# Kernel tuning notes

Measured on AMD Instinct MI355X. Metric: run time of the kernel, lower is better.

Reference implementation:

```python
import jax, jax.numpy as jnp
import numpy as np

D_MODEL = 1024
NUM_EXPERTS = 8
TOP_K = 2
B, S = 1, 2048


def setup_inputs() -> dict:
    key = jax.random.key(0)
    ks = jax.random.split(key, 8)
    sd = 1.0 / np.sqrt(D_MODEL)
    x = jax.random.normal(ks[0], (B, S, D_MODEL), dtype=jnp.float32)
    gate_w = jax.random.normal(ks[1], (D_MODEL, NUM_EXPERTS), dtype=jnp.float32) * sd
    gate_b = jnp.zeros((NUM_EXPERTS,), dtype=jnp.float32)
    w1 = jax.random.normal(ks[2], (NUM_EXPERTS, D_MODEL, 8 * D_MODEL), dtype=jnp.float32) * sd
    b1 = jnp.zeros((NUM_EXPERTS, 8 * D_MODEL), dtype=jnp.float32)
    w2 = jax.random.normal(ks[3], (NUM_EXPERTS, 4 * D_MODEL, D_MODEL), dtype=jnp.float32) * (1.0 / np.sqrt(4 * D_MODEL))
    b2 = jnp.zeros((NUM_EXPERTS, D_MODEL), dtype=jnp.float32)
    return {"x": x, "gate_w": gate_w, "gate_b": gate_b, "w1": w1, "b1": b1, "w2": w2, "b2": b2}


def reference(x, gate_w, gate_b, w1, b1, w2, b2):
    # Gating: top-k logits, softmax over the selected k
    gate_logits = jnp.einsum('bsd,de->bse', x, gate_w) + gate_b          # [B,S,E]
    weights, indices = jax.lax.top_k(gate_logits, TOP_K)                  # [B,S,K]
    weights = jax.nn.softmax(weights, axis=-1)

    # Dense all-expert compute (matches original masked-sum math; dropout in eval)
    h = jnp.einsum('bsd,edh->ebsh', x, w1) + b1[:, None, None, :]         # [E,B,S,8D]
    xh, gh = jnp.split(h, 2, axis=-1)                                     # each [E,B,S,4D]
    act = jax.nn.silu(gh) * xh
    out_e = jnp.einsum('ebsf,efd->ebsd', act, w2) + b2[:, None, None, :]  # [E,B,S,D]

    # Combine: gather the top-k expert outputs per token and weight-sum
    out_e = jnp.transpose(out_e, (1, 2, 0, 3))                            # [B,S,E,D]
    sel = jnp.take_along_axis(out_e, indices[..., None], axis=2)          # [B,S,K,D]
    return jnp.sum(sel * weights[..., None], axis=2)                      # [B,S,D]
```

## Files before the change

kernel.cpp:

```cpp
#include <hip/hip_runtime.h>
#include <hip/hip_bf16.h>

#define S 2048
#define D 1024
#define NE 8
#define HF 4096
#define HH 8192
#define BK 32
#define ACT_ROWS 4224
#define MAXRB 40

typedef __attribute__((ext_vector_type(8))) __bf16 bf16x8;
typedef __attribute__((ext_vector_type(4))) float f32x4;

__device__ __forceinline__ unsigned cvtpk(float lo, float hi) {
  unsigned r;
  asm("v_cvt_pk_bf16_f32 %0, %1, %2" : "=v"(r) : "v"(lo), "v"(hi));
  return r;
}
__device__ __forceinline__ unsigned bf16b(float f) {
  unsigned b = __float_as_uint(f);
  return (b + 0x7fffu + ((b >> 16) & 1u)) >> 16;
}
__device__ __forceinline__ void gll16(const ushort* g, ushort* l) {
  __builtin_amdgcn_global_load_lds(
      (const __attribute__((address_space(1))) void*)g,
      (__attribute__((address_space(3))) void*)l, 16, 0, 0);
}

__global__ __launch_bounds__(256) void gate_kernel(
    const float* __restrict__ x, const float* __restrict__ gw,
    const float* __restrict__ gb, ushort* __restrict__ xb,
    int* __restrict__ mi0, int* __restrict__ mi1,
    float* __restrict__ mw0, float* __restrict__ mw1) {
  const int t = blockIdx.x;
  const int l = threadIdx.x;
  const float4 xv = ((const float4*)(x + (size_t)t * D))[l];
  uint2 wv = {cvtpk(xv.x, xv.y), cvtpk(xv.z, xv.w)};
  ((uint2*)(xb + (size_t)t * D))[l] = wv;

  float xa[4] = {xv.x, xv.y, xv.z, xv.w};
  float acc[NE];
#pragma unroll
  for (int e = 0; e < NE; ++e) acc[e] = 0.f;
  const float* g0 = gw + (size_t)(4 * l) * NE;
#pragma unroll
  for (int j = 0; j < 4; ++j)
#pragma unroll
    for (int e = 0; e < NE; ++e) acc[e] += xa[j] * g0[j * NE + e];
#pragma unroll
  for (int e = 0; e < NE; ++e) {
    float v = acc[e];
#pragma unroll
    for (int off = 32; off > 0; off >>= 1) v += __shfl_xor(v, off);
    acc[e] = v;
  }
  __shared__ float sm[4][NE];
  const int wid = l >> 6;
  if ((l & 63) == 0) {
#pragma unroll
    for (int e = 0; e < NE; ++e) sm[wid][e] = acc[e];
  }
  __syncthreads();
  if (l == 0) {
    float lg[NE];
#pragma unroll
    for (int e = 0; e < NE; ++e)
      lg[e] = sm[0][e] + sm[1][e] + sm[2][e] + sm[3][e] + gb[e];
    int i0 = 0; float m0 = lg[0];
#pragma unroll
    for (int e = 1; e < NE; ++e) if (lg[e] > m0) { m0 = lg[e]; i0 = e; }
    int i1 = -1; float m1 = -3.4e38f;
#pragma unroll
    for (int e = 0; e < NE; ++e) if (e != i0 && lg[e] > m1) { m1 = lg[e]; i1 = e; }
    float p = __expf(m1 - m0);
    float inv = 1.f / (1.f + p);
    mi0[t] = i0; mi1[t] = i1;
    mw0[t] = inv; mw1[t] = p * inv;
  }
}

__global__ __launch_bounds__(1024) void route_kernel(
    const int* __restrict__ mi0, const int* __restrict__ mi1,
    int* __restrict__ counts, int* __restrict__ basep, int* __restrict__ list_tok,
    int* __restrict__ mr0, int* __restrict__ mr1,
    int* __restrict__ rb_e, int* __restrict__ rb_row0, int* __restrict__ rb_n) {
  __shared__ int cnt[NE];
  __shared__ int cur[NE];
  const int t = threadIdx.x;
  if (t < NE) cnt[t] = 0;
  __syncthreads();
  const int e0a = mi0[t], e1a = mi1[t];
  const int e0b = mi0[t + 1024], e1b = mi1[t + 1024];
  atomicAdd(&cnt[e0a], 1); atomicAdd(&cnt[e1a], 1);
  atomicAdd(&cnt[e0b], 1); atomicAdd(&cnt[e1b], 1);
  __syncthreads();
  if (t == 0) {
    int s = 0;
#pragma unroll
    for (int e = 0; e < NE; ++e) { basep[e] = s; cur[e] = s; s += cnt[e]; }
    basep[NE] = s;
    int nrb = 0;
    for (int e = 0; e < NE; ++e)
      for (int r0 = 0; r0 < cnt[e]; r0 += 128) {
        rb_e[nrb] = e; rb_row0[nrb] = r0; ++nrb;
      }
    *rb_n = nrb;
  }
  if (t < NE) counts[t] = cnt[t];
  __syncthreads();
  int r;
  r = atomicAdd(&cur[e0a], 1); list_tok[r] = t; mr0[t] = r;
  r = atomicAdd(&cur[e1a], 1); list_tok[r] = t; mr1[t] = r;
  r = atomicAdd(&cur[e0b], 1); list_tok[r] = t + 1024; mr0[t + 1024] = r;
  r = atomicAdd(&cur[e1b], 1); list_tok[r] = t + 1024; mr1[t + 1024] = r;
}

__global__ __launch_bounds__(256) void gemm1_kernel(
    const ushort* __restrict__ xb, const float* __restrict__ w1,
    const float* __restrict__ b1, const int* __restrict__ counts,
    const int* __restrict__ basep, const int* __restrict__ list_tok,
    const int* __restrict__ rb_e, const int* __restrict__ rb_row0,
    const int* __restrict__ rb_n, ushort* __restrict__ act_buf) {
  const int rb = blockIdx.y;
  if (rb >= *rb_n) return;
  const int e = rb_e[rb];
  const int row0 = rb_row0[rb];
  const int cnt = counts[e];
  const int jt = blockIdx.x * 64;
  const float* __restrict__ Wf = w1 + (size_t)e * D * HH;
  const int gbase = basep[e];

  __shared__ ushort As[2][128][BK];
  __shared__ unsigned Bs[2][32][68];

  const int tid = threadIdx.x;
  const int w = tid >> 6;
  const int i = tid & 63;

  const int rA0 = w * 32 + (i >> 2);
  const int rA1 = rA0 + 16;
  int s0 = row0 + rA0; if (s0 >= cnt) s0 = cnt - 1;
  int s1 = row0 + rA1; if (s1 >= cnt) s1 = cnt - 1;
  const ushort* pa0 = xb + (size_t)list_tok[gbase + s0] * D + (i & 3) * 8;
  const ushort* pa1 = xb + (size_t)list_tok[gbase + s1] * D + (i & 3) * 8;

  const int kp = tid >> 4;
  const int n4 = (tid & 15) * 4;
  const float* pBx = Wf + (size_t)(2 * kp) * HH + jt + n4;
  const float* pBg = pBx + HF;

  const int wm = (w >> 1) * 64;
  const int wn = (w & 1) * 32;
  const int lr = i & 15;
  const int kg = i >> 4;

  f32x4 acc[2][4][2] = {};

  {
    float4 x0 = *(const float4*)(pBx);
    float4 x1 = *(const float4*)(pBx + HH);
    float4 g0 = *(const float4*)(pBg);
    float4 g1 = *(const float4*)(pBg + HH);
    uint4 ux = {cvtpk(x0.x, x1.x), cvtpk(x0.y, x1.y), cvtpk(x0.z, x1.z), cvtpk(x0.w, x1.w)};
    uint4 ug = {cvtpk(g0.x, g1.x), cvtpk(g0.y, g1.y), cvtpk(g0.z, g1.z), cvtpk(g0.w, g1.w)};
    *(uint4*)&Bs[0][kp][n4] = ux;
    *(uint4*)&Bs[0][16 + kp][n4] = ug;
  }
  gll16(pa0, &As[0][w * 32][0]);
  gll16(pa1, &As[0][w * 32 + 16][0]);
  __syncthreads();

  int cur = 0;
#pragma unroll 1
  for (int it = 0; it < D / BK; ++it) {
    const bool pf = (it + 1 < D / BK);
    float4 x0, x1, g0, g1;
    if (pf) {
      const size_t koff = (size_t)(it + 1) * BK * HH;
      x0 = *(const float4*)(pBx + koff);
      x1 = *(const float4*)(pBx + koff + HH);
      g0 = *(const float4*)(pBg + koff);
      g1 = *(const float4*)(pBg + koff + HH);
      const int ko = (it + 1) * BK;
      gll16(pa0 + ko, &As[cur ^ 1][w * 32][0]);
      gll16(pa1 + ko, &As[cur ^ 1][w * 32 + 16][0]);
    }
    bf16x8 af[4], bfr[2][2];
#pragma unroll
    for (int mi = 0; mi < 4; ++mi)
      af[mi] = *(const bf16x8*)&As[cur][wm + mi * 16 + lr][kg * 8];
#pragma unroll
    for (int h = 0; h < 2; ++h)
#pragma unroll
      for (int ni = 0; ni < 2; ++ni) {
        const int col = wn + ni * 16 + lr;
        uint4 tv;
        tv.x = Bs[cur][h * 16 + kg * 4 + 0][col];
        tv.y = Bs[cur][h * 16 + kg * 4 + 1][col];
        tv.z = Bs[cur][h * 16 + kg * 4 + 2][col];
        tv.w = Bs[cur][h * 16 + kg * 4 + 3][col];
        bfr[h][ni] = *(const bf16x8*)&tv;
      }
#pragma unroll
    for (int h = 0; h < 2; ++h)
#pragma unroll
      for (int mi = 0; mi < 4; ++mi)
#pragma unroll
        for (int ni = 0; ni < 2; ++ni)
          acc[h][mi][ni] = __builtin_amdgcn_mfma_f32_16x16x32_bf16(af[mi], bfr[h][ni],
                                                                   acc[h][mi][ni], 0, 0, 0);
    if (pf) {
      uint4 ux = {cvtpk(x0.x, x1.x), cvtpk(x0.y, x1.y), cvtpk(x0.z, x1.z), cvtpk(x0.w, x1.w)};
      uint4 ug = {cvtpk(g0.x, g1.x), cvtpk(g0.y, g1.y), cvtpk(g0.z, g1.z), cvtpk(g0.w, g1.w)};
      *(uint4*)&Bs[cur ^ 1][kp][n4] = ux;
      *(uint4*)&Bs[cur ^ 1][16 + kp][n4] = ug;
    }
    __syncthreads();
    cur ^= 1;
  }

#pragma unroll
  for (int mi = 0; mi < 4; ++mi)
#pragma unroll
    for (int ni = 0; ni < 2; ++ni) {
      const int c = jt + wn + ni * 16 + lr;
      const float bx = b1[(size_t)e * HH + c];
      const float bg = b1[(size_t)e * HH + HF + c];
      f32x4 vx = acc[0][mi][ni];
      f32x4 vg = acc[1][mi][ni];
#pragma unroll
      for (int q = 0; q < 4; ++q) {
        const int slot = row0 + wm + mi * 16 + kg * 4 + q;
        if (slot < cnt) {
          float xv = vx[q] + bx;
          float g = vg[q] + bg;
          float a = g / (1.f + __expf(-g)) * xv;
          act_buf[(size_t)(gbase + slot) * HF + c] = (ushort)bf16b(a);
        }
      }
    }
}

__global__ __launch_bounds__(256) void gemm2_kernel(
    const ushort* __restrict__ act_buf, const float* __restrict__ w2,
    const int* __restrict__ counts, const int* __restrict__ basep,
    const int* __restrict__ rb_e, const int* __restrict__ rb_row0,
    const int* __restrict__ rb_n, ushort* __restrict__ oe) {
  const int rb = blockIdx.y;
  if (rb >= *rb_n) return;
  const int e = rb_e[rb];
  const int row0 = rb_row0[rb];
  const int cnt = counts[e];
  const int split = blockIdx.z;
  const int jt = blockIdx.x * 128;
  const float* __restrict__ Wf = w2 + (size_t)e * HF * D;
  const int gbase = basep[e];
  const size_t kbase = (size_t)split * (HF / 2);

  __shared__ ushort As[2][128][BK];
  __shared__ unsigned Bs[2][16][132];

  const int tid = threadIdx.x;
  const int w = tid >> 6;
  const int i = tid & 63;

  const int rA0 = w * 32 + (i >> 2);
  const ushort* pa0 = act_buf + (size_t)(gbase + row0 + rA0) * HF + kbase + (i & 3) * 8;
  const ushort* pa1 = pa0 + (size_t)16 * HF;

  const int grp = tid >> 5;
  const int n4 = (tid & 31) * 4;
  const float* pB0 = Wf + (kbase + 2 * grp) * D + jt + n4;
  const float* pB1 = pB0 + (size_t)16 * D;

  const int wm = (w >> 1) * 64;
  const int wn = (w & 1) * 64;
  const int lr = i & 15;
  const int kg = i >> 4;

  f32x4 acc[4][4] = {};

  {
    float4 a0 = *(const float4*)(pB0);
    float4 a1 = *(const float4*)(pB0 + D);
    float4 c0 = *(const float4*)(pB1);
    float4 c1 = *(const float4*)(pB1 + D);
    uint4 u0 = {cvtpk(a0.x, a1.x), cvtpk(a0.y, a1.y), cvtpk(a0.z, a1.z), cvtpk(a0.w, a1.w)};
    uint4 u1 = {cvtpk(c0.x, c1.x), cvtpk(c0.y, c1.y), cvtpk(c0.z, c1.z), cvtpk(c0.w, c1.w)};
    *(uint4*)&Bs[0][grp][n4] = u0;
    *(uint4*)&Bs[0][8 + grp][n4] = u1;
  }
  gll16(pa0, &As[0][w * 32][0]);
  gll16(pa1, &As[0][w * 32 + 16][0]);
  __syncthreads();

  int cur = 0;
#pragma unroll 1
  for (int it = 0; it < (HF / 2) / BK; ++it) {
    const bool pf = (it + 1 < (HF / 2) / BK);
    float4 a0, a1, c0, c1;
    if (pf) {
      const size_t koff = (size_t)(it + 1) * BK * D;
      a0 = *(const float4*)(pB0 + koff);
      a1 = *(const float4*)(pB0 + koff + D);
      c0 = *(const float4*)(pB1 + koff);
      c1 = *(const float4*)(pB1 + koff + D);
      const int ko = (it + 1) * BK;
      gll16(pa0 + ko, &As[cur ^ 1][w * 32][0]);
      gll16(pa1 + ko, &As[cur ^ 1][w * 32 + 16][0]);
    }
    bf16x8 af[4], bfr[4];
#pragma unroll
    for (int mi = 0; mi < 4; ++mi)
      af[mi] = *(const bf16x8*)&As[cur][wm + mi * 16 + lr][kg * 8];
#pragma unroll
    for (int ni = 0; ni < 4; ++ni) {
      const int col = wn + ni * 16 + lr;
      uint4 tv;
      tv.x = Bs[cur][kg * 4 + 0][col];
      tv.y = Bs[cur][kg * 4 + 1][col];
      tv.z = Bs[cur][kg * 4 + 2][col];
      tv.w = Bs[cur][kg * 4 + 3][col];
      bfr[ni] = *(const bf16x8*)&tv;
    }
#pragma unroll
    for (int mi = 0; mi < 4; ++mi)
#pragma unroll
      for (int ni = 0; ni < 4; ++ni)
        acc[mi][ni] = __builtin_amdgcn_mfma_f32_16x16x32_bf16(af[mi], bfr[ni],
                                                              acc[mi][ni], 0, 0, 0);
    if (pf) {
      uint4 u0 = {cvtpk(a0.x, a1.x), cvtpk(a0.y, a1.y), cvtpk(a0.z, a1.z), cvtpk(a0.w, a1.w)};
      uint4 u1 = {cvtpk(c0.x, c1.x), cvtpk(c0.y, c1.y), cvtpk(c0.z, c1.z), cvtpk(c0.w, c1.w)};
      *(uint4*)&Bs[cur ^ 1][grp][n4] = u0;
      *(uint4*)&Bs[cur ^ 1][8 + grp][n4] = u1;
    }
    __syncthreads();
    cur ^= 1;
  }

#pragma unroll
  for (int mi = 0; mi < 4; ++mi)
#pragma unroll
    for (int ni = 0; ni < 4; ++ni) {
      f32x4 v = acc[mi][ni];
#pragma unroll
      for (int q = 0; q < 4; ++q) {
        const int slot = row0 + wm + mi * 16 + kg * 4 + q;
        if (slot < cnt)
          oe[((size_t)split * ACT_ROWS + gbase + slot) * D + jt + wn + ni * 16 + lr] =
              (ushort)bf16b(v[q]);
      }
    }
}

__global__ void combine_kernel(const ushort* __restrict__ oe,
                               const int* __restrict__ mr0, const int* __restrict__ mr1,
                               const float* __restrict__ mw0, const float* __restrict__ mw1,
                               const int* __restrict__ mi0, const int* __restrict__ mi1,
                               const float* __restrict__ b2, float* __restrict__ out) {
  const int t = blockIdx.x;
  const int l = threadIdx.x;
  const float w0 = mw0[t], w1 = mw1[t];
  const int r0 = mr0[t], r1 = mr1[t];
  float a0[4] = {0.f, 0.f, 0.f, 0.f}, a1[4] = {0.f, 0.f, 0.f, 0.f};
#pragma unroll
  for (int s = 0; s < 2; ++s) {
    uint2 u0 = *(const uint2*)(oe + ((size_t)s * ACT_ROWS + r0) * D + l * 4);
    uint2 u1 = *(const uint2*)(oe + ((size_t)s * ACT_ROWS + r1) * D + l * 4);
    a0[0] += __uint_as_float(u0.x << 16);
    a0[1] += __uint_as_float(u0.x & 0xffff0000u);
    a0[2] += __uint_as_float(u0.y << 16);
    a0[3] += __uint_as_float(u0.y & 0xffff0000u);
    a1[0] += __uint_as_float(u1.x << 16);
    a1[1] += __uint_as_float(u1.x & 0xffff0000u);
    a1[2] += __uint_as_float(u1.y << 16);
    a1[3] += __uint_as_float(u1.y & 0xffff0000u);
  }
  float4 c0 = ((const float4*)(b2 + (size_t)mi0[t] * D))[l];
  float4 c1 = ((const float4*)(b2 + (size_t)mi1[t] * D))[l];
  float4 r;
  r.x = w0 * (a0[0] + c0.x) + w1 * (a1[0] + c1.x);
  r.y = w0 * (a0[1] + c0.y) + w1 * (a1[1] + c1.y);
  r.z = w0 * (a0[2] + c0.z) + w1 * (a1[2] + c1.z);
  r.w = w0 * (a0[3] + c0.w) + w1 * (a1[3] + c1.w);
  ((float4*)(out + (size_t)t * D))[l] = r;
}

extern "C" void kernel_launch(void* const* d_in, const int* in_sizes, int n_in,
                              void* d_out, int out_size, void* d_ws, size_t ws_size,
                              hipStream_t stream) {
  const float* x  = (const float*)d_in[0];
  const float* gw = (const float*)d_in[1];
  const float* gb = (const float*)d_in[2];
  const float* w1 = (const float*)d_in[3];
  const float* b1 = (const float*)d_in[4];
  const float* w2 = (const float*)d_in[5];
  const float* b2 = (const float*)d_in[6];
  float* out = (float*)d_out;

  char* ws = (char*)d_ws;
  int*   counts   = (int*)(ws + 0);
  int*   basep    = (int*)(ws + 64);
  int*   rb_n     = (int*)(ws + 128);
  int*   rb_e     = (int*)(ws + 192);
  int*   rb_row0  = (int*)(ws + 384);
  int*   mi0      = (int*)(ws + 1024);
  int*   mi1      = (int*)(ws + 1024 + 1 * 8192);
  int*   mr0      = (int*)(ws + 1024 + 2 * 8192);
  int*   mr1      = (int*)(ws + 1024 + 3 * 8192);
  float* mw0      = (float*)(ws + 1024 + 4 * 8192);
  float* mw1      = (float*)(ws + 1024 + 5 * 8192);
  int*   list_tok = (int*)(ws + 1024 + 6 * 8192);
  ushort* xb      = (ushort*)(ws + 66560);
  ushort* act_buf = (ushort*)(ws + 4260864);
  ushort* oe      = (ushort*)(ws + 38863872);

  gate_kernel<<<S, 256, 0, stream>>>(x, gw, gb, xb, mi0, mi1, mw0, mw1);
  route_kernel<<<1, 1024, 0, stream>>>(mi0, mi1, counts, basep, list_tok, mr0, mr1,
                                       rb_e, rb_row0, rb_n);
  gemm1_kernel<<<dim3(64, MAXRB), 256, 0, stream>>>(xb, w1, b1, counts, basep, list_tok,
                                                    rb_e, rb_row0, rb_n, act_buf);
  gemm2_kernel<<<dim3(8, MAXRB, 2), 256, 0, stream>>>(act_buf, w2, counts, basep,
                                                      rb_e, rb_row0, rb_n, oe);
  combine_kernel<<<S, 256, 0, stream>>>(oe, mr0, mr1, mw0, mw1, mi0, mi1, b2, out);
}
```

Before: 266.1 us.

## Enlarge gemm1 row tile to 256 with 512 threads to halve weight re-reads

Routes gemm1 through a second row-block list with 256-row blocks and launches it with 512 threads, so each block covers twice as many token rows per expert. Each w1 fp32 tile is loaded and converted to bf16 once per 256 rows instead of once per 128, and the B-tile load is split so each half of the threads handles either the x or the gate half. This is meant to cut redundant global weight traffic and conversion work. In exchange the grid has fewer blocks, LDS per block grows, and experts with few tokens pad more rows per block.

New measurement: 261.4 us (median of 2 runs). No clear change (-1.8%).

```diff
diff --git a/kernel.cpp b/kernel.cpp
--- a/kernel.cpp
+++ b/kernel.cpp
@@ -9,6 +9,7 @@
 #define BK 32
 #define ACT_ROWS 4224
 #define MAXRB 40
+#define MAXRB2 24
 
 typedef __attribute__((ext_vector_type(8))) __bf16 bf16x8;
 typedef __attribute__((ext_vector_type(4))) float f32x4;
@@ -84,7 +85,8 @@
     const int* __restrict__ mi0, const int* __restrict__ mi1,
     int* __restrict__ counts, int* __restrict__ basep, int* __restrict__ list_tok,
     int* __restrict__ mr0, int* __restrict__ mr1,
-    int* __restrict__ rb_e, int* __restrict__ rb_row0, int* __restrict__ rb_n) {
+    int* __restrict__ rb_e, int* __restrict__ rb_row0, int* __restrict__ rb_n,
+    int* __restrict__ rb2_e, int* __restrict__ rb2_row0, int* __restrict__ rb2_n) {
   __shared__ int cnt[NE];
   __shared__ int cur[NE];
   const int t = threadIdx.x;
@@ -100,12 +102,17 @@
 #pragma unroll
     for (int e = 0; e < NE; ++e) { basep[e] = s; cur[e] = s; s += cnt[e]; }
     basep[NE] = s;
-    int nrb = 0;
-    for (int e = 0; e < NE; ++e)
+    int nrb = 0, nrb2 = 0;
+    for (int e = 0; e < NE; ++e) {
       for (int r0 = 0; r0 < cnt[e]; r0 += 128) {
         rb_e[nrb] = e; rb_row0[nrb] = r0; ++nrb;
       }
+      for (int r0 = 0; r0 < cnt[e]; r0 += 256) {
+        rb2_e[nrb2] = e; rb2_row0[nrb2] = r0; ++nrb2;
+      }
+    }
     *rb_n = nrb;
+    *rb2_n = nrb2;
   }
   if (t < NE) counts[t] = cnt[t];
   __syncthreads();
@@ -116,22 +123,22 @@
   r = atomicAdd(&cur[e1b], 1); list_tok[r] = t + 1024; mr1[t + 1024] = r;
 }
 
-__global__ __launch_bounds__(256) void gemm1_kernel(
+__global__ __launch_bounds__(512) void gemm1_kernel(
     const ushort* __restrict__ xb, const float* __restrict__ w1,
     const float* __restrict__ b1, const int* __restrict__ counts,
     const int* __restrict__ basep, const int* __restrict__ list_tok,
-    const int* __restrict__ rb_e, const int* __restrict__ rb_row0,
-    const int* __restrict__ rb_n, ushort* __restrict__ act_buf) {
+    const int* __restrict__ rb2_e, const int* __restrict__ rb2_row0,
+    const int* __restrict__ rb2_n, ushort* __restrict__ act_buf) {
   const int rb = blockIdx.y;
-  if (rb >= *rb_n) return;
-  const int e = rb_e[rb];
-  const int row0 = rb_row0[rb];
+  if (rb >= *rb2_n) return;
+  const int e = rb2_e[rb];
+  const int row0 = rb2_row0[rb];
   const int cnt = counts[e];
   const int jt = blockIdx.x * 64;
   const float* __restrict__ Wf = w1 + (size_t)e * D * HH;
   const int gbase = basep[e];
 
-  __shared__ ushort As[2][128][BK];
+  __shared__ ushort As[2][256][BK];
   __shared__ unsigned Bs[2][32][68];
 
   const int tid = threadIdx.x;
@@ -145,10 +152,10 @@
   const ushort* pa0 = xb + (size_t)list_tok[gbase + s0] * D + (i & 3) * 8;
   const ushort* pa1 = xb + (size_t)list_tok[gbase + s1] * D + (i & 3) * 8;
 
-  const int kp = tid >> 4;
+  const int half = tid >> 8;
+  const int kp = (tid >> 4) & 15;
   const int n4 = (tid & 15) * 4;
-  const float* pBx = Wf + (size_t)(2 * kp) * HH + jt + n4;
-  const float* pBg = pBx + HF;
+  const float* pB = Wf + (size_t)(2 * kp) * HH + jt + n4 + half * HF;
 
   const int wm = (w >> 1) * 64;
   const int wn = (w & 1) * 32;
@@ -158,14 +165,11 @@
   f32x4 acc[2][4][2] = {};
 
   {
-    float4 x0 = *(const float4*)(pBx);
-    float4 x1 = *(const float4*)(pBx + HH);
-    float4 g0 = *(const float4*)(pBg);
-    float4 g1 = *(const float4*)(pBg + HH);
-    uint4 ux = {cvtpk(x0.x, x1.x), cvtpk(x0.y, x1.y), cvtpk(x0.z, x1.z), cvtpk(x0.w, x1.w)};
-    uint4 ug = {cvtpk(g0.x, g1.x), cvtpk(g0.y, g1.y), cvtpk(g0.z, g1.z), cvtpk(g0.w, g1.w)};
-    *(uint4*)&Bs[0][kp][n4] = ux;
-    *(uint4*)&Bs[0][16 + kp][n4] = ug;
+    float4 b0v = *(const float4*)(pB);
+    float4 b1v = *(const float4*)(pB + HH);
+    uint4 u = {cvtpk(b0v.x, b1v.x), cvtpk(b0v.y, b1v.y),
+               cvtpk(b0v.z, b1v.z), cvtpk(b0v.w, b1v.w)};
+    *(uint4*)&Bs[0][half * 16 + kp][n4] = u;
   }
   gll16(pa0, &As[0][w * 32][0]);
   gll16(pa1, &As[0][w * 32 + 16][0]);
@@ -175,13 +179,11 @@
 #pragma unroll 1
   for (int it = 0; it < D / BK; ++it) {
     const bool pf = (it + 1 < D / BK);
-    float4 x0, x1, g0, g1;
+    float4 b0v, b1v;
     if (pf) {
       const size_t koff = (size_t)(it + 1) * BK * HH;
-      x0 = *(const float4*)(pBx + koff);
-      x1 = *(const float4*)(pBx + koff + HH);
-      g0 = *(const float4*)(pBg + koff);
-      g1 = *(const float4*)(pBg + koff + HH);
+      b0v = *(const float4*)(pB + koff);
+      b1v = *(const float4*)(pB + koff + HH);
       const int ko = (it + 1) * BK;
       gll16(pa0 + ko, &As[cur ^ 1][w * 32][0]);
       gll16(pa1 + ko, &As[cur ^ 1][w * 32 + 16][0]);
@@ -211,10 +213,9 @@
           acc[h][mi][ni] = __builtin_amdgcn_mfma_f32_16x16x32_bf16(af[mi], bfr[h][ni],
                                                                    acc[h][mi][ni], 0, 0, 0);
     if (pf) {
-      uint4 ux = {cvtpk(x0.x, x1.x), cvtpk(x0.y, x1.y), cvtpk(x0.z, x1.z), cvtpk(x0.w, x1.w)};
-      uint4 ug = {cvtpk(g0.x, g1.x), cvtpk(g0.y, g1.y), cvtpk(g0.z, g1.z), cvtpk(g0.w, g1.w)};
-      *(uint4*)&Bs[cur ^ 1][kp][n4] = ux;
-      *(uint4*)&Bs[cur ^ 1][16 + kp][n4] = ug;
+      uint4 u = {cvtpk(b0v.x, b1v.x), cvtpk(b0v.y, b1v.y),
+                 cvtpk(b0v.z, b1v.z), cvtpk(b0v.w, b1v.w)};
+      *(uint4*)&Bs[cur ^ 1][half * 16 + kp][n4] = u;
     }
     __syncthreads();
     cur ^= 1;
@@ -406,6 +407,9 @@
   int*   rb_n     = (int*)(ws + 128);
   int*   rb_e     = (int*)(ws + 192);
   int*   rb_row0  = (int*)(ws + 384);
+  int*   rb2_n    = (int*)(ws + 576);
+  int*   rb2_e    = (int*)(ws + 640);
+  int*   rb2_row0 = (int*)(ws + 768);
   int*   mi0      = (int*)(ws + 1024);
   int*   mi1      = (int*)(ws + 1024 + 1 * 8192);
   int*   mr0      = (int*)(ws + 1024 + 2 * 8192);
@@ -419,9 +423,9 @@
 
   gate_kernel<<<S, 256, 0, stream>>>(x, gw, gb, xb, mi0, mi1, mw0, mw1);
   route_kernel<<<1, 1024, 0, stream>>>(mi0, mi1, counts, basep, list_tok, mr0, mr1,
-                                       rb_e, rb_row0, rb_n);
-  gemm1_kernel<<<dim3(64, MAXRB), 256, 0, stream>>>(xb, w1, b1, counts, basep, list_tok,
-                                                    rb_e, rb_row0, rb_n, act_buf);
+                                       rb_e, rb_row0, rb_n, rb2_e, rb2_row0, rb2_n);
+  gemm1_kernel<<<dim3(64, MAXRB2), 512, 0, stream>>>(xb, w1, b1, counts, basep, list_tok,
+                                                     rb2_e, rb2_row0, rb2_n, act_buf);
   gemm2_kernel<<<dim3(8, MAXRB, 2), 256, 0, stream>>>(act_buf, w2, counts, basep,
                                                       rb_e, rb_row0, rb_n, oe);
   combine_kernel<<<S, 256, 0, stream>>>(oe, mr0, mr1, mw0, mw1, mi0, mi1, b2, out);
```
